# Performance work log

Hardware: AMD Instinct MI355X
Metric: run time of the kernel (lower is better)

## Reference

```python
import jax, jax.numpy as jnp
import numpy as np


def _box_filter(img):
    # img: [B,1,H,W]; 5x5 uniform kernel, padding=4 -> output [B,1,H+4,W+4]
    k = jnp.full((1, 1, 5, 5), 1.0 / 25.0, dtype=img.dtype)
    return jax.lax.conv_general_dilated(
        img, k, window_strides=(1, 1), padding=((4, 4), (4, 4)),
        dimension_numbers=('NCHW', 'OIHW', 'NCHW'))


def setup_inputs() -> dict:
    key = jax.random.key(0)
    k1, k2 = jax.random.split(key)
    x = jax.random.normal(k1, (64, 1, 512, 512), dtype=jnp.float32)
    y = jax.random.normal(k2, (64, 1, 512, 512), dtype=jnp.float32)
    return {"x": x, "y": y}


def reference(x, y):
    diff = _box_filter(x) - _box_filter(y)
    # faithful to torch.mean(torch.sqrt(diff * diff)) (== mean(|diff|))
    return jnp.mean(jnp.sqrt(diff * diff))
```

## Files before the change

### kernel.cpp

```cpp
#include <hip/hip_runtime.h>


#define TR      12
#define STRIPS  43
#define NBLOCKS ((STRIPS * 64) / 4)
#define NROWS   (TR + 4)

__global__ __launch_bounds__(256) void box_loss_kernel(
    const float* __restrict__ x, const float* __restrict__ y,
    float* __restrict__ ws, float* __restrict__ out)
{
    __shared__ float wsum[4];

    const int lane  = threadIdx.x & 63;
    const int wid   = (blockIdx.x << 2) + (threadIdx.x >> 6);
    const int img   = wid / STRIPS;
    const int s0    = wid - img * STRIPS;
    const int strip = (s0 + img * 17) % STRIPS;
    const int i0    = strip * TR;

    const size_t base = (size_t)img * (512 * 512) + (size_t)(lane * 8);
    const float* xb = x + base;
    const float* yb = y + base;

    float4 px[4][2], py[4][2];

    #pragma unroll
    for (int k = 0; k < 4; ++k) {
        const int r  = i0 - 4 + k;
        const int rc = min(max(r, 0), 511);
        const float4* xr = (const float4*)(xb + (size_t)rc * 512);
        const float4* yr = (const float4*)(yb + (size_t)rc * 512);
        px[k][0] = xr[0]; px[k][1] = xr[1];
        py[k][0] = yr[0]; py[k][1] = yr[1];
    }
    __builtin_amdgcn_sched_barrier(0);

    float hist[5][8], v[8];
    #pragma unroll
    for (int j = 0; j < 8; ++j) v[j] = 0.f;
    #pragma unroll
    for (int s = 0; s < 5; ++s)
        #pragma unroll
        for (int j = 0; j < 8; ++j) hist[s][j] = 0.f;

    float acc = 0.f;

    #pragma unroll
    for (int k = 0; k < NROWS; ++k) {
        const int st = k & 3;
        float4 xa = px[st][0], xc = px[st][1];
        float4 ya = py[st][0], yc = py[st][1];

        if (k + 4 < NROWS) {
            const int r  = i0 - 4 + (k + 4);
            const int rc = min(max(r, 0), 511);
            const float4* xr = (const float4*)(xb + (size_t)rc * 512);
            const float4* yr = (const float4*)(yb + (size_t)rc * 512);
            px[st][0] = xr[0]; px[st][1] = xr[1];
            py[st][0] = yr[0]; py[st][1] = yr[1];
        }
        __builtin_amdgcn_sched_barrier(0);

        const int r = i0 - 4 + k;
        const bool valid = (r >= 0) & (r < 512);
        float d[8];
        d[0] = xa.x - ya.x; d[1] = xa.y - ya.y; d[2] = xa.z - ya.z; d[3] = xa.w - ya.w;
        d[4] = xc.x - yc.x; d[5] = xc.y - yc.y; d[6] = xc.z - yc.z; d[7] = xc.w - yc.w;
        #pragma unroll
        for (int j = 0; j < 8; ++j) d[j] = valid ? d[j] : 0.f;

        const int slot = k % 5;
        #pragma unroll
        for (int j = 0; j < 8; ++j) {
            v[j] += d[j] - hist[slot][j];
            hist[slot][j] = d[j];
        }

        if (k >= 4) {
            float h0 = __shfl_up(v[4], 1, 64);
            float h1 = __shfl_up(v[5], 1, 64);
            float h2 = __shfl_up(v[6], 1, 64);
            float h3 = __shfl_up(v[7], 1, 64);
            if (lane == 0) { h0 = 0.f; h1 = 0.f; h2 = 0.f; h3 = 0.f; }

            float s = h0 + h1 + h2 + h3 + v[0];
            acc += fabsf(s);
            s += v[1] - h0;   acc += fabsf(s);
            s += v[2] - h1;   acc += fabsf(s);
            s += v[3] - h2;   acc += fabsf(s);
            s += v[4] - h3;   acc += fabsf(s);
            s += v[5] - v[0]; acc += fabsf(s);
            s += v[6] - v[1]; acc += fabsf(s);
            s += v[7] - v[2]; acc += fabsf(s);
            if (lane == 63) {
                float q = v[7];  acc += fabsf(q);
                q += v[6];       acc += fabsf(q);
                q += v[5];       acc += fabsf(q);
                q += v[4];       acc += fabsf(q);
            }
        }
    }

    #pragma unroll
    for (int off = 32; off > 0; off >>= 1)
        acc += __shfl_down(acc, off, 64);
    if (lane == 0) wsum[threadIdx.x >> 6] = acc;
    __syncthreads();

    if (threadIdx.x == 0) {
        float s = wsum[0] + wsum[1] + wsum[2] + wsum[3];
        atomicAdd(ws, s);
        __threadfence();
        unsigned* cnt = (unsigned*)(ws + 1);
        unsigned done = atomicAdd(cnt, 1u);
        if (done == (unsigned)(gridDim.x - 1)) {
            float total = atomicAdd(ws, 0.0f);
            out[0] = total * (1.0f / (25.0f * 64.0f * 516.0f * 516.0f));
        }
    }
}

extern "C" void kernel_launch(void* const* d_in, const int* in_sizes, int n_in,
                              void* d_out, int out_size, void* d_ws, size_t ws_size,
                              hipStream_t stream) {
    const float* x = (const float*)d_in[0];
    const float* y = (const float*)d_in[1];
    float* out = (float*)d_out;
    float* ws  = (float*)d_ws;

    hipMemsetAsync(ws, 0, 8, stream);

    box_loss_kernel<<<NBLOCKS, 256, 0, stream>>>(x, y, ws, out);
}
```

Baseline: 178.1 us.

## Use persistent blocks with atomic band queue and direct global-to-LDS loads

Replaces the fixed one-strip-per-wave grid with 512 persistent blocks whose waves pull 12-row bands from an atomic counter. Row loads now go straight into a 4-slot per-wave LDS ring through global_load_lds, paced by explicit vmcnt waits with three rows in flight. This is meant to cut register pressure and tail imbalance and to keep more loads outstanding. In exchange it adds one atomic per band, LDS reads, and depends on hand-counted vmcnt values being correct.

After: 198.1 us. 1.11x slower.

```diff
diff --git a/kernel.cpp b/kernel.cpp
--- a/kernel.cpp
+++ b/kernel.cpp
@@ -1,120 +1,137 @@
 #include <hip/hip_runtime.h>
 
 
-#define TR      12
-#define STRIPS  43
-#define NBLOCKS ((STRIPS * 64) / 4)
-#define NROWS   (TR + 4)
+#define TRB            12
+#define BANDS_PER_IMG  43
+#define TOTAL_BANDS    (BANDS_PER_IMG * 64)
+#define NROWS          (TRB + 4)
+#define NBLOCKS        512
+
+typedef __attribute__((address_space(1))) const void glb_t;
+typedef __attribute__((address_space(3))) void lds_t;
 
 __global__ __launch_bounds__(256) void box_loss_kernel(
     const float* __restrict__ x, const float* __restrict__ y,
     float* __restrict__ ws, float* __restrict__ out)
 {
+    __shared__ float lds[4][4][1024];
     __shared__ float wsum[4];
 
-    const int lane  = threadIdx.x & 63;
-    const int wid   = (blockIdx.x << 2) + (threadIdx.x >> 6);
-    const int img   = wid / STRIPS;
-    const int s0    = wid - img * STRIPS;
-    const int strip = (s0 + img * 17) % STRIPS;
-    const int i0    = strip * TR;
+    const int lane = threadIdx.x & 63;
+    const int w    = threadIdx.x >> 6;
+    float* const wlds = &lds[w][0][0];
 
-    const size_t base = (size_t)img * (512 * 512) + (size_t)(lane * 8);
-    const float* xb = x + base;
-    const float* yb = y + base;
+    unsigned* bandctr = (unsigned*)ws + 1;
+    unsigned* donectr = (unsigned*)ws + 2;
 
-    float4 px[4][2], py[4][2];
-
-    #pragma unroll
-    for (int k = 0; k < 4; ++k) {
-        const int r  = i0 - 4 + k;
-        const int rc = min(max(r, 0), 511);
-        const float4* xr = (const float4*)(xb + (size_t)rc * 512);
-        const float4* yr = (const float4*)(yb + (size_t)rc * 512);
-        px[k][0] = xr[0]; px[k][1] = xr[1];
-        py[k][0] = yr[0]; py[k][1] = yr[1];
-    }
-    __builtin_amdgcn_sched_barrier(0);
-
-    float hist[5][8], v[8];
-    #pragma unroll
-    for (int j = 0; j < 8; ++j) v[j] = 0.f;
-    #pragma unroll
-    for (int s = 0; s < 5; ++s)
-        #pragma unroll
-        for (int j = 0; j < 8; ++j) hist[s][j] = 0.f;
+    const int loff = lane * 4;
 
     float acc = 0.f;
 
-    #pragma unroll
-    for (int k = 0; k < NROWS; ++k) {
-        const int st = k & 3;
-        float4 xa = px[st][0], xc = px[st][1];
-        float4 ya = py[st][0], yc = py[st][1];
+    for (;;) {
+        unsigned id;
+        if (lane == 0) id = atomicAdd(bandctr, 1u);
+        id = (unsigned)__shfl((int)id, 0, 64);
+        if (id >= TOTAL_BANDS) break;
 
-        if (k + 4 < NROWS) {
-            const int r  = i0 - 4 + (k + 4);
-            const int rc = min(max(r, 0), 511);
-            const float4* xr = (const float4*)(xb + (size_t)rc * 512);
-            const float4* yr = (const float4*)(yb + (size_t)rc * 512);
-            px[st][0] = xr[0]; px[st][1] = xr[1];
-            py[st][0] = yr[0]; py[st][1] = yr[1];
+        const int img  = (int)(id / BANDS_PER_IMG);
+        const int band = (int)(id - (unsigned)img * BANDS_PER_IMG);
+        const int i0   = band * TRB;
+
+        const float* xb = x + (size_t)img * (512 * 512);
+        const float* yb = y + (size_t)img * (512 * 512);
+
+        #define ISSUE_ROW(k) do {                                                        \
+            const int rc_ = min(max(i0 - 4 + (k), 0), 511);                              \
+            const float* gx_ = xb + (size_t)rc_ * 512 + loff;                            \
+            const float* gy_ = yb + (size_t)rc_ * 512 + loff;                            \
+            float* lb_ = wlds + ((k) & 3) * 1024;                                        \
+            __builtin_amdgcn_global_load_lds((glb_t*)(gx_),       (lds_t*)(lb_),       16, 0, 0); \
+            __builtin_amdgcn_global_load_lds((glb_t*)(gx_ + 256), (lds_t*)(lb_ + 256), 16, 0, 0); \
+            __builtin_amdgcn_global_load_lds((glb_t*)(gy_),       (lds_t*)(lb_ + 512), 16, 0, 0); \
+            __builtin_amdgcn_global_load_lds((glb_t*)(gy_ + 256), (lds_t*)(lb_ + 768), 16, 0, 0); \
+        } while (0)
+
+        ISSUE_ROW(0); ISSUE_ROW(1); ISSUE_ROW(2);
+
+        float hist[5][8], v[8];
+        #pragma unroll
+        for (int j = 0; j < 8; ++j) v[j] = 0.f;
+        #pragma unroll
+        for (int s = 0; s < 5; ++s)
+            #pragma unroll
+            for (int j = 0; j < 8; ++j) hist[s][j] = 0.f;
+
+        #pragma unroll
+        for (int k = 0; k < NROWS; ++k) {
+            if (k + 3 < NROWS) ISSUE_ROW(k + 3);
+
+            if      (k < NROWS - 3)  asm volatile("s_waitcnt vmcnt(12)" ::: "memory");
+            else if (k == NROWS - 3) asm volatile("s_waitcnt vmcnt(8)"  ::: "memory");
+            else if (k == NROWS - 2) asm volatile("s_waitcnt vmcnt(4)"  ::: "memory");
+            else                     asm volatile("s_waitcnt vmcnt(0)"  ::: "memory");
+
+            const float* sl = wlds + (k & 3) * 1024;
+            const float4 xa = *(const float4*)(sl + lane * 8);
+            const float4 xc = *(const float4*)(sl + lane * 8 + 4);
+            const float4 ya = *(const float4*)(sl + 512 + lane * 8);
+            const float4 yc = *(const float4*)(sl + 512 + lane * 8 + 4);
+
+            const int r = i0 - 4 + k;
+            const bool valid = (r >= 0) & (r < 512);
+            float d[8];
+            d[0] = xa.x - ya.x; d[1] = xa.y - ya.y; d[2] = xa.z - ya.z; d[3] = xa.w - ya.w;
+            d[4] = xc.x - yc.x; d[5] = xc.y - yc.y; d[6] = xc.z - yc.z; d[7] = xc.w - yc.w;
+            #pragma unroll
+            for (int j = 0; j < 8; ++j) d[j] = valid ? d[j] : 0.f;
+
+            const int s5 = k % 5;
+            #pragma unroll
+            for (int j = 0; j < 8; ++j) {
+                v[j] += d[j] - hist[s5][j];
+                hist[s5][j] = d[j];
+            }
+
+            if (k >= 4) {
+                float h0 = __shfl_up(v[4], 1, 64);
+                float h1 = __shfl_up(v[5], 1, 64);
+                float h2 = __shfl_up(v[6], 1, 64);
+                float h3 = __shfl_up(v[7], 1, 64);
+                if (lane == 0) { h0 = 0.f; h1 = 0.f; h2 = 0.f; h3 = 0.f; }
+
+                float s = h0 + h1 + h2 + h3 + v[0];
+                acc += fabsf(s);
+                s += v[1] - h0;   acc += fabsf(s);
+                s += v[2] - h1;   acc += fabsf(s);
+                s += v[3] - h2;   acc += fabsf(s);
+                s += v[4] - h3;   acc += fabsf(s);
+                s += v[5] - v[0]; acc += fabsf(s);
+                s += v[6] - v[1]; acc += fabsf(s);
+                s += v[7] - v[2]; acc += fabsf(s);
+                if (lane == 63) {
+                    float q = v[7];  acc += fabsf(q);
+                    q += v[6];       acc += fabsf(q);
+                    q += v[5];       acc += fabsf(q);
+                    q += v[4];       acc += fabsf(q);
+                }
+            }
+            asm volatile("" ::: "memory");
         }
-        __builtin_amdgcn_sched_barrier(0);
-
-        const int r = i0 - 4 + k;
-        const bool valid = (r >= 0) & (r < 512);
-        float d[8];
-        d[0] = xa.x - ya.x; d[1] = xa.y - ya.y; d[2] = xa.z - ya.z; d[3] = xa.w - ya.w;
-        d[4] = xc.x - yc.x; d[5] = xc.y - yc.y; d[6] = xc.z - yc.z; d[7] = xc.w - yc.w;
-        #pragma unroll
-        for (int j = 0; j < 8; ++j) d[j] = valid ? d[j] : 0.f;
-
-        const int slot = k % 5;
-        #pragma unroll
-        for (int j = 0; j < 8; ++j) {
-            v[j] += d[j] - hist[slot][j];
-            hist[slot][j] = d[j];
-        }
-
-        if (k >= 4) {
-            float h0 = __shfl_up(v[4], 1, 64);
-            float h1 = __shfl_up(v[5], 1, 64);
-            float h2 = __shfl_up(v[6], 1, 64);
-            float h3 = __shfl_up(v[7], 1, 64);
-            if (lane == 0) { h0 = 0.f; h1 = 0.f; h2 = 0.f; h3 = 0.f; }
-
-            float s = h0 + h1 + h2 + h3 + v[0];
-            acc += fabsf(s);
-            s += v[1] - h0;   acc += fabsf(s);
-            s += v[2] - h1;   acc += fabsf(s);
-            s += v[3] - h2;   acc += fabsf(s);
-            s += v[4] - h3;   acc += fabsf(s);
-            s += v[5] - v[0]; acc += fabsf(s);
-            s += v[6] - v[1]; acc += fabsf(s);
-            s += v[7] - v[2]; acc += fabsf(s);
-            if (lane == 63) {
-                float q = v[7];  acc += fabsf(q);
-                q += v[6];       acc += fabsf(q);
-                q += v[5];       acc += fabsf(q);
-                q += v[4];       acc += fabsf(q);
-            }
-        }
+        #undef ISSUE_ROW
     }
 
     #pragma unroll
     for (int off = 32; off > 0; off >>= 1)
         acc += __shfl_down(acc, off, 64);
-    if (lane == 0) wsum[threadIdx.x >> 6] = acc;
+    if (lane == 0) wsum[w] = acc;
     __syncthreads();
 
     if (threadIdx.x == 0) {
         float s = wsum[0] + wsum[1] + wsum[2] + wsum[3];
         atomicAdd(ws, s);
         __threadfence();
-        unsigned* cnt = (unsigned*)(ws + 1);
-        unsigned done = atomicAdd(cnt, 1u);
-        if (done == (unsigned)(gridDim.x - 1)) {
+        unsigned done = atomicAdd(donectr, 1u);
+        if (done == (unsigned)(NBLOCKS - 1)) {
             float total = atomicAdd(ws, 0.0f);
             out[0] = total * (1.0f / (25.0f * 64.0f * 516.0f * 516.0f));
         }
@@ -129,7 +146,7 @@
     float* out = (float*)d_out;
     float* ws  = (float*)d_ws;
 
-    hipMemsetAsync(ws, 0, 8, stream);
+    hipMemsetAsync(ws, 0, 12, stream);
 
     box_loss_kernel<<<NBLOCKS, 256, 0, stream>>>(x, y, ws, out);
 }
```
